# Kernel optimization log

Measured on AMD Instinct MI355X. Metric: run time of the kernel, lower is better.

## Reference

```python
import jax, jax.numpy as jnp
import numpy as np

EPS = 1e-6


def setup_inputs() -> dict:
    key = jax.random.key(0)
    k1, k2 = jax.random.split(key)
    B, Lq, Lk, D = 16, 1024, 1024, 512
    query = jax.random.normal(k1, (B, Lq, D), dtype=jnp.float32)
    context = jax.random.normal(k2, (B, Lk, D), dtype=jnp.float32)
    gamma = jnp.ones((D,), dtype=jnp.float32)
    beta = jnp.zeros((D,), dtype=jnp.float32)
    return {"query": query, "context": context, "gamma": gamma, "beta": beta}


def _layer_norm(x, gamma, beta):
    mean = jnp.mean(x, axis=-1, keepdims=True)
    var = jnp.var(x, axis=-1, keepdims=True)
    return gamma * (x - mean) * jax.lax.rsqrt(var + EPS) + beta


def reference(query, context, gamma, beta):
    # query: [B, Lq, D], context: [B, Lk, D]
    D = query.shape[-1]
    scale = 1.0 / np.sqrt(D).astype(np.float32)
    # additive-style tanh-activated scores: [B, Lq, Lk]
    score = jnp.tanh(jnp.einsum('bqd,bkd->bqk', query, context) * scale)
    attn = jax.nn.softmax(score, axis=2)
    # dropout is identity in eval/reference mode
    out = jnp.einsum('bqk,bkd->bqd', attn, context)
    out = _layer_norm(out + query, gamma, beta)
    return out
```

## Files before the change

### kernel.cpp

```cpp
#include <hip/hip_runtime.h>
#include <hip/hip_bf16.h>
#include <cstdint>

#define LQ 1024
#define LK 1024
#define DD 512
#define NB 16
#define QB 64
#define KB 32
#define NT (LK / KB)

typedef short bf16x8 __attribute__((ext_vector_type(8)));
typedef float f32x4 __attribute__((ext_vector_type(4)));

__device__ __forceinline__ uint16_t f2bf(float f) {
  uint32_t u = __builtin_bit_cast(uint32_t, f);
  u = (u + 0x7fffu + ((u >> 16) & 1u)) >> 16;
  return (uint16_t)u;
}

__device__ __forceinline__ void load_lds16(const void* g, void* l) {
  __builtin_amdgcn_global_load_lds(
      (const __attribute__((address_space(1))) uint32_t*)g,
      (__attribute__((address_space(3))) uint32_t*)l, 16, 0, 0);
}

__global__ __launch_bounds__(256) void prep_kernel(const float* __restrict__ c,
                                                   uint16_t* __restrict__ cb,
                                                   uint16_t* __restrict__ ct) {
  __shared__ float t[32][33];
  const int k0 = blockIdx.x * 32, d0 = blockIdx.y * 32, b = blockIdx.z;
  const float* src = c + (size_t)b * LK * DD;
  uint16_t* cbd = cb + (size_t)b * LK * DD;
  uint16_t* ctd = ct + (size_t)b * DD * LK;
  const int tx = threadIdx.x, ty = threadIdx.y;
  for (int j = 0; j < 4; ++j) {
    int k = ty + j * 8;
    float v = src[(size_t)(k0 + k) * DD + d0 + tx];
    t[k][tx] = v;
    cbd[(size_t)(k0 + k) * DD + d0 + tx] = f2bf(v);
  }
  __syncthreads();
  for (int j = 0; j < 4; ++j) {
    int d = ty + j * 8;
    ctd[(size_t)(d0 + d) * LK + k0 + tx] = f2bf(t[tx][d]);
  }
}

__global__ __launch_bounds__(512, 2) void attn_kernel(
    const uint16_t* __restrict__ Cb, const uint16_t* __restrict__ Ctb,
    const float* __restrict__ Qf, const float* __restrict__ gamma,
    const float* __restrict__ beta, float* __restrict__ out) {
  __shared__ char cs[2][32 * 1024];
  __shared__ char cts[2][32 * 1024];
  __shared__ char plds[64 * 80];
  __shared__ float denom_s[64];
  __shared__ float rsum_s[64], rsumsq_s[64], mean_s[64], rstd_s[64];

  const int tid = threadIdx.x;
  const int w = tid >> 6, l = tid & 63, c = l & 15, g = l >> 4;
  const int orig = blockIdx.x;
  const int virt = ((orig & 7) << 5) | (orig >> 3);
  const int b = virt >> 4, qblk = virt & 15;
  const int q0 = qblk * QB;
  const int mt = w & 1, qt = w >> 1;
  const float scale = 0.044194173824159216f;

  if (tid < 64) { denom_s[tid] = 0.f; rsum_s[tid] = 0.f; rsumsq_s[tid] = 0.f; }

  bf16x8 qfrag[16];
  {
    const float* qrow = Qf + ((size_t)b * LQ + q0 + qt * 16 + c) * DD;
    for (int s = 0; s < 16; ++s) {
      float4 a0 = *(const float4*)(qrow + s * 32 + g * 8);
      float4 a1 = *(const float4*)(qrow + s * 32 + g * 8 + 4);
      ushort4 u0, u1;
      u0.x = f2bf(a0.x); u0.y = f2bf(a0.y); u0.z = f2bf(a0.z); u0.w = f2bf(a0.w);
      u1.x = f2bf(a1.x); u1.y = f2bf(a1.y); u1.z = f2bf(a1.z); u1.w = f2bf(a1.w);
      union { ushort4 u[2]; bf16x8 v; } pk;
      pk.u[0] = u0; pk.u[1] = u1;
      qfrag[s] = pk.v;
    }
  }

  f32x4 oacc[4][4];
  for (int i = 0; i < 4; ++i)
    for (int j = 0; j < 4; ++j) oacc[i][j] = (f32x4){0.f, 0.f, 0.f, 0.f};
  float dacc = 0.f;

  const char* cbyte = (const char*)Cb + (size_t)b * LK * DD * 2;
  const char* ctbyte = (const char*)Ctb + (size_t)b * DD * LK * 2;

  auto stage = [&](int buf, int kt2) {
    const int kk0 = kt2 * KB;
    for (int j = 0; j < 4; ++j) {
      int r = w * 4 + j;
      const char* src = cbyte + (size_t)(kk0 + r) * 1024 + ((l * 16) ^ ((r & 7) << 4));
      load_lds16(src, cs[buf] + r * 1024);
    }
    for (int j = 0; j < 4; ++j) {
      int d0l = w * 64 + j * 16;
      int d = d0l + (l >> 2);
      const char* src =
          ctbyte + (size_t)d * 2048 + kk0 * 2 + (((l & 3) * 16) ^ ((d & 3) << 4));
      load_lds16(src, cts[buf] + d0l * 64);
    }
  };

  stage(0, 0);
  __syncthreads();

  for (int kt = 0; kt < NT; ++kt) {
    const int cur = kt & 1;
    if (kt + 1 < NT) stage(cur ^ 1, kt + 1);

    f32x4 sacc = {0.f, 0.f, 0.f, 0.f};
    {
      const int kkA = mt * 16 + c;
      const int swz = (kkA & 7) << 4;
      const char* arow = cs[cur] + kkA * 1024;
      for (int s = 0; s < 16; ++s) {
        bf16x8 a = *(const bf16x8*)(arow + ((s * 64 + g * 16) ^ swz));
        sacc = __builtin_amdgcn_mfma_f32_16x16x32_bf16(a, qfrag[s], sacc, 0, 0, 0);
      }
    }
    {
      float pv[4];
      for (int i = 0; i < 4; ++i) {
        float sv = sacc[i] * scale;
        float e2 = __expf(2.f * sv);
        float th = (e2 - 1.f) / (e2 + 1.f);
        float p = __expf(th);
        pv[i] = p;
        dacc += p;
      }
      uint32_t p01 = ((uint32_t)f2bf(pv[1]) << 16) | f2bf(pv[0]);
      uint32_t p23 = ((uint32_t)f2bf(pv[3]) << 16) | f2bf(pv[2]);
      char* pr = plds + (qt * 16 + c) * 80 + (mt * 16 + g * 4) * 2;
      *(uint32_t*)pr = p01;
      *(uint32_t*)(pr + 4) = p23;
    }
    asm volatile("s_waitcnt lgkmcnt(0)" ::: "memory");
    __builtin_amdgcn_s_barrier();
    __builtin_amdgcn_sched_barrier(0);

    bf16x8 pa[4], pb[4];
    for (int q2 = 0; q2 < 4; ++q2)
      pa[q2] = *(const bf16x8*)(plds + (q2 * 16 + c) * 80 + g * 16);
    for (int nt = 0; nt < 4; ++nt) {
      int d = w * 64 + nt * 16 + c;
      pb[nt] = *(const bf16x8*)(cts[cur] + d * 64 + ((g * 16) ^ ((d & 3) << 4)));
    }
    for (int q2 = 0; q2 < 4; ++q2)
      for (int nt = 0; nt < 4; ++nt)
        oacc[q2][nt] =
            __builtin_amdgcn_mfma_f32_16x16x32_bf16(pa[q2], pb[nt], oacc[q2][nt], 0, 0, 0);

    __syncthreads();
  }

  float dv = dacc;
  dv += __shfl_xor(dv, 16);
  dv += __shfl_xor(dv, 32);
  if (l < 16) atomicAdd(&denom_s[qt * 16 + l], dv);
  __syncthreads();

  const float* qsrc = Qf + ((size_t)b * LQ + q0) * DD;
  for (int q2 = 0; q2 < 4; ++q2)
    for (int i = 0; i < 4; ++i) {
      int row = q2 * 16 + g * 4 + i;
      float inv = 1.f / denom_s[row];
      for (int nt = 0; nt < 4; ++nt) {
        int d = w * 64 + nt * 16 + c;
        float o = oacc[q2][nt][i] * inv + qsrc[(size_t)row * DD + d];
        oacc[q2][nt][i] = o;
      }
    }
  for (int q2 = 0; q2 < 4; ++q2)
    for (int i = 0; i < 4; ++i) {
      float s1 = 0.f, s2 = 0.f;
      for (int nt = 0; nt < 4; ++nt) {
        float v = oacc[q2][nt][i];
        s1 += v;
        s2 += v * v;
      }
      s1 += __shfl_xor(s1, 1); s2 += __shfl_xor(s2, 1);
      s1 += __shfl_xor(s1, 2); s2 += __shfl_xor(s2, 2);
      s1 += __shfl_xor(s1, 4); s2 += __shfl_xor(s2, 4);
      s1 += __shfl_xor(s1, 8); s2 += __shfl_xor(s2, 8);
      if (c == 0) {
        int row = q2 * 16 + g * 4 + i;
        atomicAdd(&rsum_s[row], s1);
        atomicAdd(&rsumsq_s[row], s2);
      }
    }
  __syncthreads();
  if (tid < 64) {
    float m = rsum_s[tid] * (1.f / DD);
    float var = rsumsq_s[tid] * (1.f / DD) - m * m;
    mean_s[tid] = m;
    rstd_s[tid] = rsqrtf(fmaxf(var, 0.f) + 1e-6f);
  }
  __syncthreads();
  float* op = out + ((size_t)b * LQ + q0) * DD;
  for (int q2 = 0; q2 < 4; ++q2)
    for (int i = 0; i < 4; ++i) {
      int row = q2 * 16 + g * 4 + i;
      float m = mean_s[row], r = rstd_s[row];
      for (int nt = 0; nt < 4; ++nt) {
        int d = w * 64 + nt * 16 + c;
        op[(size_t)row * DD + d] = gamma[d] * ((oacc[q2][nt][i] - m) * r) + beta[d];
      }
    }
}

__global__ __launch_bounds__(256) void naive_kernel(const float* __restrict__ Q,
                                                    const float* __restrict__ C,
                                                    const float* __restrict__ gamma,
                                                    const float* __restrict__ beta,
                                                    float* __restrict__ out) {
  const int row = blockIdx.x;
  const int b = row >> 10;
  const int tid = threadIdx.x;
  __shared__ float qs[DD];
  __shared__ float ps[LK];
  __shared__ float ys[DD];
  __shared__ float red[256];
  const float* qp = Q + (size_t)row * DD;
  const float* cb = C + (size_t)b * LK * DD;
  for (int d = tid; d < DD; d += 256) qs[d] = qp[d];
  __syncthreads();
  for (int k = tid; k < LK; k += 256) {
    const float* cr = cb + (size_t)k * DD;
    float s = 0.f;
    for (int d = 0; d < DD; ++d) s += qs[d] * cr[d];
    s *= 0.044194173824159216f;
    float e2 = __expf(2.f * s);
    float th = (e2 - 1.f) / (e2 + 1.f);
    ps[k] = __expf(th);
  }
  __syncthreads();
  float dsum = 0.f;
  for (int k = tid; k < LK; k += 256) dsum += ps[k];
  red[tid] = dsum;
  __syncthreads();
  for (int off = 128; off; off >>= 1) {
    if (tid < off) red[tid] += red[tid + off];
    __syncthreads();
  }
  float inv = 1.f / red[0];
  __syncthreads();
  for (int d = tid; d < DD; d += 256) {
    float o = 0.f;
    for (int k = 0; k < LK; ++k) o += ps[k] * cb[(size_t)k * DD + d];
    ys[d] = o * inv + qs[d];
  }
  __syncthreads();
  float s1 = 0.f;
  for (int d = tid; d < DD; d += 256) s1 += ys[d];
  red[tid] = s1;
  __syncthreads();
  for (int off = 128; off; off >>= 1) {
    if (tid < off) red[tid] += red[tid + off];
    __syncthreads();
  }
  float mean = red[0] * (1.f / DD);
  __syncthreads();
  float s2 = 0.f;
  for (int d = tid; d < DD; d += 256) {
    float v = ys[d] - mean;
    s2 += v * v;
  }
  red[tid] = s2;
  __syncthreads();
  for (int off = 128; off; off >>= 1) {
    if (tid < off) red[tid] += red[tid + off];
    __syncthreads();
  }
  float rstd = rsqrtf(red[0] * (1.f / DD) + 1e-6f);
  for (int d = tid; d < DD; d += 256)
    out[(size_t)row * DD + d] = gamma[d] * ((ys[d] - mean) * rstd) + beta[d];
}

extern "C" void kernel_launch(void* const* d_in, const int* in_sizes, int n_in,
                              void* d_out, int out_size, void* d_ws, size_t ws_size,
                              hipStream_t stream) {
  const float* Qf = (const float*)d_in[0];
  const float* Cf = (const float*)d_in[1];
  const float* gamma = (const float*)d_in[2];
  const float* beta = (const float*)d_in[3];
  float* out = (float*)d_out;
  const size_t nelem = (size_t)NB * LK * DD;
  const size_t need = nelem * 2 * 2;
  if (ws_size >= need) {
    uint16_t* Cb = (uint16_t*)d_ws;
    uint16_t* Ctb = Cb + nelem;
    prep_kernel<<<dim3(LK / 32, DD / 32, NB), dim3(32, 8), 0, stream>>>(Cf, Cb, Ctb);
    attn_kernel<<<256, 512, 0, stream>>>(Cb, Ctb, Qf, gamma, beta, out);
  } else {
    naive_kernel<<<NB * LQ, 256, 0, stream>>>(Qf, Cf, gamma, beta, out);
  }
}
```

Baseline: 87.15 us.

## Software-pipeline PV matmul one tile behind and load transposed context directly to registers

Restructures the attention loop so the P·V MFMA for tile kt-1 runs in the same phase as the score MFMA for tile kt. This removes one of the two barriers per iteration, and the P staging buffer is double-buffered to allow it. The transposed-context operand is now read straight from global memory into registers, prefetched one tile ahead, instead of being staged in LDS. The context tile uses a padded row stride with a simpler swizzle. It also uses s_setprio around the MFMA blocks and a hardware reciprocal in tanh. LDS use drops, but register pressure rises and the global loads of the transposed tile are not coalesced.

```diff
diff --git a/kernel.cpp b/kernel.cpp
--- a/kernel.cpp
+++ b/kernel.cpp
@@ -9,6 +9,7 @@
 #define QB 64
 #define KB 32
 #define NT (LK / KB)
+#define CSTRIDE 1088
 
 typedef short bf16x8 __attribute__((ext_vector_type(8)));
 typedef float f32x4 __attribute__((ext_vector_type(4)));
@@ -51,9 +52,8 @@
     const uint16_t* __restrict__ Cb, const uint16_t* __restrict__ Ctb,
     const float* __restrict__ Qf, const float* __restrict__ gamma,
     const float* __restrict__ beta, float* __restrict__ out) {
-  __shared__ char cs[2][32 * 1024];
-  __shared__ char cts[2][32 * 1024];
-  __shared__ char plds[64 * 80];
+  __shared__ uint4 cs4[2][32 * CSTRIDE / 16];
+  __shared__ char plds[2][64 * 80];
   __shared__ float denom_s[64];
   __shared__ float rsum_s[64], rsumsq_s[64], mean_s[64], rstd_s[64];
 
@@ -83,6 +83,10 @@
     }
   }
 
+  const int kkA = mt * 16 + c;
+  const char* arow0 = (const char*)cs4[0] + kkA * CSTRIDE + ((g ^ (kkA & 3)) * 16);
+  const char* arow1 = (const char*)cs4[1] + kkA * CSTRIDE + ((g ^ (kkA & 3)) * 16);
+
   f32x4 oacc[4][4];
   for (int i = 0; i < 4; ++i)
     for (int j = 0; j < 4; ++j) oacc[i][j] = (f32x4){0.f, 0.f, 0.f, 0.f};
@@ -91,72 +95,92 @@
   const char* cbyte = (const char*)Cb + (size_t)b * LK * DD * 2;
   const char* ctbyte = (const char*)Ctb + (size_t)b * DD * LK * 2;
 
-  auto stage = [&](int buf, int kt2) {
-    const int kk0 = kt2 * KB;
-    for (int j = 0; j < 4; ++j) {
-      int r = w * 4 + j;
-      const char* src = cbyte + (size_t)(kk0 + r) * 1024 + ((l * 16) ^ ((r & 7) << 4));
-      load_lds16(src, cs[buf] + r * 1024);
-    }
-    for (int j = 0; j < 4; ++j) {
-      int d0l = w * 64 + j * 16;
-      int d = d0l + (l >> 2);
-      const char* src =
-          ctbyte + (size_t)d * 2048 + kk0 * 2 + (((l & 3) * 16) ^ ((d & 3) << 4));
-      load_lds16(src, cts[buf] + d0l * 64);
-    }
+  int csrcoff[4];
+  for (int j = 0; j < 4; ++j) {
+    int r = w * 4 + j;
+    csrcoff[j] = r * 1024 + ((l * 16) ^ ((r & 3) << 4));
+  }
+  const char* pbbase = ctbyte + (size_t)(w * 64 + c) * 2048 + g * 16;
+
+  char* pwr0 = plds[0] + (qt * 16 + c) * 80 + (mt * 16 + g * 4) * 2;
+  char* pwr1 = plds[1] + (qt * 16 + c) * 80 + (mt * 16 + g * 4) * 2;
+  const char* par0 = plds[0] + c * 80 + g * 16;
+  const char* par1 = plds[1] + c * 80 + g * 16;
+
+  auto stageC = [&](int buf, int kt2) {
+    const char* s0 = cbyte + (size_t)kt2 * 32768;
+    char* base = (char*)cs4[buf];
+    for (int j = 0; j < 4; ++j)
+      load_lds16(s0 + csrcoff[j], base + (w * 4 + j) * CSTRIDE);
   };
-
-  stage(0, 0);
-  __syncthreads();
-
-  for (int kt = 0; kt < NT; ++kt) {
+  auto loadPB = [&](bf16x8(&pbn)[4], int kt2) {
+    const char* p = pbbase + kt2 * 64;
+    pbn[0] = *(const bf16x8*)(p);
+    pbn[1] = *(const bf16x8*)(p + 32768);
+    pbn[2] = *(const bf16x8*)(p + 65536);
+    pbn[3] = *(const bf16x8*)(p + 98304);
+  };
+
+  bf16x8 pbA[4], pbB[4];
+
+  stageC(0, 0);
+  __syncthreads();
+
+  auto body = [&](int kt, bf16x8(&pbc)[4], bf16x8(&pbn)[4]) {
     const int cur = kt & 1;
-    if (kt + 1 < NT) stage(cur ^ 1, kt + 1);
-
+    if (kt + 1 < NT) stageC(cur ^ 1, kt + 1);
+    loadPB(pbn, kt);
+    if (kt) {
+      const char* par = cur ? par0 : par1;
+      bf16x8 pa[4];
+      for (int q2 = 0; q2 < 4; ++q2) pa[q2] = *(const bf16x8*)(par + q2 * 1280);
+      __builtin_amdgcn_s_setprio(1);
+      for (int q2 = 0; q2 < 4; ++q2)
+        for (int n2 = 0; n2 < 4; ++n2)
+          oacc[q2][n2] =
+              __builtin_amdgcn_mfma_f32_16x16x32_bf16(pa[q2], pbc[n2], oacc[q2][n2], 0, 0, 0);
+      __builtin_amdgcn_s_setprio(0);
+    }
     f32x4 sacc = {0.f, 0.f, 0.f, 0.f};
     {
-      const int kkA = mt * 16 + c;
-      const int swz = (kkA & 7) << 4;
-      const char* arow = cs[cur] + kkA * 1024;
+      const char* arow = cur ? arow1 : arow0;
+      __builtin_amdgcn_s_setprio(1);
       for (int s = 0; s < 16; ++s) {
-        bf16x8 a = *(const bf16x8*)(arow + ((s * 64 + g * 16) ^ swz));
+        bf16x8 a = *(const bf16x8*)(arow + s * 64);
         sacc = __builtin_amdgcn_mfma_f32_16x16x32_bf16(a, qfrag[s], sacc, 0, 0, 0);
       }
+      __builtin_amdgcn_s_setprio(0);
     }
     {
       float pv[4];
       for (int i = 0; i < 4; ++i) {
         float sv = sacc[i] * scale;
-        float e2 = __expf(2.f * sv);
-        float th = (e2 - 1.f) / (e2 + 1.f);
+        float e2 = __expf(sv * 2.f);
+        float r = __builtin_amdgcn_rcpf(e2 + 1.f);
+        float th = (e2 - 1.f) * r;
         float p = __expf(th);
         pv[i] = p;
         dacc += p;
       }
-      uint32_t p01 = ((uint32_t)f2bf(pv[1]) << 16) | f2bf(pv[0]);
-      uint32_t p23 = ((uint32_t)f2bf(pv[3]) << 16) | f2bf(pv[2]);
-      char* pr = plds + (qt * 16 + c) * 80 + (mt * 16 + g * 4) * 2;
-      *(uint32_t*)pr = p01;
-      *(uint32_t*)(pr + 4) = p23;
-    }
-    asm volatile("s_waitcnt lgkmcnt(0)" ::: "memory");
-    __builtin_amdgcn_s_barrier();
-    __builtin_amdgcn_sched_barrier(0);
-
-    bf16x8 pa[4], pb[4];
+      uint2 pk;
+      pk.x = ((uint32_t)f2bf(pv[1]) << 16) | f2bf(pv[0]);
+      pk.y = ((uint32_t)f2bf(pv[3]) << 16) | f2bf(pv[2]);
+      *(uint2*)(cur ? pwr1 : pwr0) = pk;
+    }
+    __syncthreads();
+  };
+
+  for (int kt = 0; kt < NT; kt += 2) {
+    body(kt, pbB, pbA);
+    body(kt + 1, pbA, pbB);
+  }
+  {
+    bf16x8 pa[4];
+    for (int q2 = 0; q2 < 4; ++q2) pa[q2] = *(const bf16x8*)(par1 + q2 * 1280);
     for (int q2 = 0; q2 < 4; ++q2)
-      pa[q2] = *(const bf16x8*)(plds + (q2 * 16 + c) * 80 + g * 16);
-    for (int nt = 0; nt < 4; ++nt) {
-      int d = w * 64 + nt * 16 + c;
-      pb[nt] = *(const bf16x8*)(cts[cur] + d * 64 + ((g * 16) ^ ((d & 3) << 4)));
-    }
-    for (int q2 = 0; q2 < 4; ++q2)
-      for (int nt = 0; nt < 4; ++nt)
-        oacc[q2][nt] =
-            __builtin_amdgcn_mfma_f32_16x16x32_bf16(pa[q2], pb[nt], oacc[q2][nt], 0, 0, 0);
-
-    __syncthreads();
+      for (int n2 = 0; n2 < 4; ++n2)
+        oacc[q2][n2] =
+            __builtin_amdgcn_mfma_f32_16x16x32_bf16(pa[q2], pbB[n2], oacc[q2][n2], 0, 0, 0);
   }
 
   float dv = dacc;
```

Result: slower. 95.72 us (+9.8%).
